# Kernel tuning notes

Measured on AMD Instinct MI355X. Metric: run time of the kernel, lower is better.

The kernel has to match this reference:

```python
import jax, jax.numpy as jnp
import numpy as np

B, DIRS, C, H, W = 2, 64, 630, 128, 128

def setup_inputs() -> dict:
    key = jax.random.key(0)
    k1, k2, k3, k4, k5 = jax.random.split(key, 5)
    theta_global = jax.random.normal(k1, (B, 4, H, W), dtype=jnp.float32) * 0.1
    theta_dir = jax.random.normal(k2, (B, DIRS, 6, H, W), dtype=jnp.float32) * 0.1
    t_vec = jax.random.uniform(k3, (C,), dtype=jnp.float32)
    b_vec = jax.random.uniform(k4, (C,), dtype=jnp.float32)
    P = jax.random.normal(k5, (C, DIRS), dtype=jnp.float32) * 0.1
    return {"theta_global": theta_global, "theta_dir": theta_dir,
            "t_vec": t_vec, "b_vec": b_vec, "P": P}

def _log_s(theta_global, theta_dir, t_vec, b_vec, P):
    ln_s0 = theta_global[:, 0:1]   # [B,1,H,W]
    r = theta_global[:, 1:2]
    sigma20 = theta_global[:, 2:3]
    sigma30 = theta_global[:, 3:4]
    # project all six direction-coefficient maps at once: [B,6,C,H,W]
    proj = jnp.einsum('cd,bdkhw->bkchw', P, theta_dir)
    D_ch, s11, s02, s21, s12, s03 = (proj[:, k] for k in range(6))
    t = t_vec.reshape(1, -1, 1, 1)  # [1,C,1,1]
    b = b_vec.reshape(1, -1, 1, 1)
    t2, b2, tb = t * t, b * b, t * b
    t3, b3, t2b, tb2 = t2 * t, b2 * b, t2 * b, t * b2
    log_s = (ln_s0 - r * t - D_ch * b
             + 0.5 * (sigma20 * t2 + 2.0 * s11 * tb + s02 * b2)
             - (1.0 / 6.0) * (sigma30 * t3 + 3.0 * s21 * t2b + 3.0 * s12 * tb2 + s03 * b3))
    return log_s

def reference(theta_global, theta_dir, t_vec, b_vec, P):
    return jnp.exp(_log_s(theta_global, theta_dir, t_vec, b_vec, P))
```

## Files before the change

### kernel.cpp

```cpp
#include <hip/hip_runtime.h>
#include <math.h>

#define BATCH 2
#define NDIRS 64
#define NCH   630
#define MPAD  640
#define HW    16384
#define KDIR  384
#define NT    12
#define PANEL 64
#define NPOSW 5
#define NITER (NPOSW * NT)
#define BROWE 392

#define BS_OFF 0
#define AS_OFF 50176
#define TV_OFF 74752
#define TG_OFF 77312
#define LDS_TOTAL 78336

typedef float f32x4 __attribute__((ext_vector_type(4)));
typedef short s16x8 __attribute__((ext_vector_type(8)));

__device__ __forceinline__ ushort f2bf(float f) {
    unsigned u = __builtin_bit_cast(unsigned, f);
    u = (u + 0x7FFFu + ((u >> 16) & 1u)) >> 16;
    return (ushort)u;
}

__device__ __forceinline__ uint cvt_pk_bf16(float lo, float hi) {
    uint r;
    asm("v_cvt_pk_bf16_f32 %0, %1, %2" : "=v"(r) : "v"(lo), "v"(hi));
    return r;
}

__device__ __forceinline__ f32x4 ntload(const float* p) {
    return __builtin_nontemporal_load((const f32x4*)p);
}

typedef const __attribute__((address_space(1))) unsigned int g_u32;
typedef __attribute__((address_space(3))) unsigned int l_u32;
__device__ __forceinline__ void gload16(const void* g, void* l) {
    __builtin_amdgcn_global_load_lds((g_u32*)g, (l_u32*)l, 16, 0, 0);
}

__global__ void prep_kernel(const float* __restrict__ t_vec,
                            const float* __restrict__ b_vec,
                            const float* __restrict__ P,
                            ushort* __restrict__ W2b) {
    int c = blockIdx.x;
    int j = threadIdx.x;
    float w = 0.0f;
    if (c < NCH) {
        int d = j / 6, k = j - d * 6;
        float t = t_vec[c];
        float bb = b_vec[c];
        float coeff;
        switch (k) {
            case 0:  coeff = -bb;                           break;
            case 1:  coeff = t * bb;                        break;
            case 2:  coeff = 0.5f * bb * bb;                break;
            case 3:  coeff = -0.5f * t * t * bb;            break;
            case 4:  coeff = -0.5f * t * bb * bb;           break;
            default: coeff = -(1.0f / 6.0f) * bb * bb * bb; break;
        }
        w = coeff * P[c * NDIRS + d];
    }
    int kstep = j >> 5, k5 = j & 31, k8 = k5 >> 3, klo = k5 & 7;
    int s = k8 ^ ((c >> 1) & 3);
    W2b[c * KDIR + kstep * 32 + s * 8 + klo] = f2bf(w);
}

__global__ __launch_bounds__(256, 2) void fused_gemm(
        const ushort* __restrict__ W2b,
        const float*  __restrict__ TD,
        const float*  __restrict__ t_vec,
        const float*  __restrict__ TG,
        float* __restrict__ out)
{
    extern __shared__ char lds[];

    const int nt_ = blockIdx.x;
    const int bz  = blockIdx.y;
    const int n0  = nt_ * PANEL;

    const int tid  = threadIdx.x;
    const int lane = tid & 63;
    const int wid  = tid >> 6;
    const int l15 = lane & 15, lhi = lane >> 4;
    const int aslot = lhi ^ ((l15 >> 1) & 3);

    ushort* bsU = (ushort*)(lds + BS_OFF);
    char*   asW = lds + AS_OFF + wid * 6144;
    float*  tvl = (float*)(lds + TV_OFF);
    float*  tgl = (float*)(lds + TG_OFF);

    tvl[tid]       = t_vec[tid];
    tvl[tid + 256] = t_vec[tid + 256];
    if (tid < NCH - 512) tvl[tid + 512] = t_vec[tid + 512];
    else if (tid + 512 < MPAD) tvl[tid + 512] = 0.0f;
    {
        int p = tid >> 6, px = tid & 63;
        tgl[p * PANEL + px] = TG[((size_t)bz * 4 + p) * HW + n0 + px];
    }

    const ushort* aB0 = W2b + (size_t)(wid * 160 + (lane >> 2)) * KDIR
                        + (lane & 3) * 8;
    const ushort* aB1 = aB0 + (size_t)16 * KDIR;
    gload16(aB0, asW);             gload16(aB1, asW + 1024);
    __builtin_amdgcn_sched_barrier(0);
    gload16(aB0 + 32, asW + 2048); gload16(aB1 + 32, asW + 3072);
    __builtin_amdgcn_sched_barrier(0);

    const int kq2 = tid >> 4;
    const int pg  = tid & 15;
    const float* bR = TD + ((size_t)bz * KDIR + 2 * kq2) * HW + n0 + pg * 4;
    const int sxor = ((kq2 >> 2) ^ (pg & 3) ^ ((pg >> 2) & 3)) & 3;
    const int wbase = (kq2 & 3) * 2;

    {
        f32x4 lo0, hi0, lo1, hi1, lo2, hi2, lo3, hi3;
        lo0 = ntload(bR);
        hi0 = ntload(bR + HW);
        lo1 = ntload(bR + (size_t)32 * HW);
        hi1 = ntload(bR + (size_t)33 * HW);
        lo2 = ntload(bR + (size_t)64 * HW);
        hi2 = ntload(bR + (size_t)65 * HW);

#define BSTEP(S, LC, HC, LN, HN)                                               \
        {                                                                      \
            if ((S) + 3 < NT) {                                                \
                LN = ntload(bR + (size_t)(((S) + 3) * 32) * HW);               \
                HN = ntload(bR + (size_t)(((S) + 3) * 32 + 1) * HW);           \
            }                                                                  \
            _Pragma("unroll")                                                  \
            for (int i = 0; i < 4; ++i) {                                      \
                uint w_ = cvt_pk_bf16(LC[i], HC[i]);                           \
                int s_ = (sxor ^ i) & 3;                                       \
                *(uint*)&bsU[(pg * 4 + i) * BROWE + (S) * 32 + s_ * 8 + wbase] = w_; \
            }                                                                  \
        }
        BSTEP(0, lo0, hi0, lo3, hi3)  BSTEP(1, lo1, hi1, lo0, hi0)
        BSTEP(2, lo2, hi2, lo1, hi1)  BSTEP(3, lo3, hi3, lo2, hi2)
        BSTEP(4, lo0, hi0, lo3, hi3)  BSTEP(5, lo1, hi1, lo0, hi0)
        BSTEP(6, lo2, hi2, lo1, hi1)  BSTEP(7, lo3, hi3, lo2, hi2)
        BSTEP(8, lo0, hi0, lo3, hi3)  BSTEP(9, lo1, hi1, lo0, hi0)
        BSTEP(10, lo2, hi2, lo1, hi1) BSTEP(11, lo3, hi3, lo2, hi2)
#undef BSTEP
    }

    asm volatile("s_waitcnt lgkmcnt(0)" ::: "memory");
    __builtin_amdgcn_s_barrier();
    __builtin_amdgcn_sched_barrier(0);

    float gg[4][4];
    #pragma unroll
    for (int n = 0; n < 4; ++n)
        #pragma unroll
        for (int p = 0; p < 4; ++p) gg[n][p] = tgl[p * PANEL + n * 16 + l15];

    f32x4 acc[2][4];
    #pragma unroll
    for (int m = 0; m < 2; ++m)
        #pragma unroll
        for (int n = 0; n < 4; ++n) acc[m][n] = (f32x4){0.f, 0.f, 0.f, 0.f};

#define ITER(G, WSTR)                                                          \
    {                                                                          \
        constexpr int T_ = (G) % NT, buf_ = (G) % 3;                           \
        constexpr int gn_ = (G) + 2;                                           \
        if constexpr (gn_ < NITER) {                                           \
            constexpr int pi_ = gn_ / NT, ti_ = gn_ % NT, nb_ = gn_ % 3;       \
            gload16(aB0 + (size_t)(pi_ * 32) * KDIR + ti_ * 32,                \
                    asW + nb_ * 2048);                                         \
            gload16(aB1 + (size_t)(pi_ * 32) * KDIR + ti_ * 32,                \
                    asW + nb_ * 2048 + 1024);                                  \
            __builtin_amdgcn_sched_barrier(0);                                 \
        }                                                                      \
        s16x8 bf[4];                                                           \
        _Pragma("unroll")                                                      \
        for (int n = 0; n < 4; ++n) {                                          \
            const int rs_ = (lhi ^ (l15 & 3) ^ ((l15 >> 2) & 3) ^ (n)) & 3;    \
            bf[n] = *(const s16x8*)&bsU[(n * 16 + l15) * BROWE + T_ * 32 + rs_ * 8]; \
        }                                                                      \
        asm volatile(WSTR ::: "memory");                                       \
        s16x8 af[2];                                                           \
        const ushort* asR = (const ushort*)(asW + buf_ * 2048);                \
        _Pragma("unroll")                                                      \
        for (int m = 0; m < 2; ++m)                                            \
            af[m] = *(const s16x8*)&asR[(m * 16 + l15) * 32 + aslot * 8];      \
        __builtin_amdgcn_s_setprio(1);                                         \
        _Pragma("unroll")                                                      \
        for (int m = 0; m < 2; ++m)                                            \
            _Pragma("unroll")                                                  \
            for (int n = 0; n < 4; ++n)                                        \
                acc[m][n] = __builtin_amdgcn_mfma_f32_16x16x32_bf16(           \
                                af[m], bf[n], acc[m][n], 0, 0, 0);             \
        __builtin_amdgcn_s_setprio(0);                                         \
    }

#define EPI(P_)                                                                \
    {                                                                          \
        _Pragma("unroll")                                                      \
        for (int m = 0; m < 2; ++m) {                                          \
            _Pragma("unroll")                                                  \
            for (int r = 0; r < 4; ++r) {                                      \
                int c = wid * 160 + (P_) * 32 + m * 16 + lhi * 4 + r;          \
                float t_ = tvl[c];                                             \
                float ct1 = -t_, ct2 = 0.5f * t_ * t_;                         \
                float ct3 = -(1.0f / 6.0f) * t_ * t_ * t_;                     \
                float* orow = out + ((size_t)bz * NCH + c) * HW + n0 + l15;    \
                _Pragma("unroll")                                              \
                for (int n = 0; n < 4; ++n) {                                  \
                    float base = gg[n][0] + ct1 * gg[n][1]                     \
                               + ct2 * gg[n][2] + ct3 * gg[n][3];              \
                    __builtin_nontemporal_store(                               \
                        __expf(acc[m][n][r] + base), orow + n * 16);           \
                }                                                              \
            }                                                                  \
        }                                                                      \
        _Pragma("unroll")                                                      \
        for (int m = 0; m < 2; ++m)                                            \
            _Pragma("unroll")                                                  \
            for (int n = 0; n < 4; ++n) acc[m][n] = (f32x4){0.f,0.f,0.f,0.f};  \
    }

#define W36 "s_waitcnt vmcnt(36)"
#define W4  "s_waitcnt vmcnt(4)"
#define W2  "s_waitcnt vmcnt(2)"
#define W0  "s_waitcnt vmcnt(0)"

    ITER(0,  W4)  ITER(1,  W4)  ITER(2,  W4)  ITER(3,  W4)  ITER(4,  W4)
    ITER(5,  W4)  ITER(6,  W4)  ITER(7,  W4)  ITER(8,  W4)  ITER(9,  W4)
    ITER(10, W4)  ITER(11, W4)
    EPI(0)
    ITER(12, W36) ITER(13, W36) ITER(14, W4)  ITER(15, W4)  ITER(16, W4)
    ITER(17, W4)  ITER(18, W4)  ITER(19, W4)  ITER(20, W4)  ITER(21, W4)
    ITER(22, W4)  ITER(23, W4)
    EPI(1)
    ITER(24, W36) ITER(25, W36) ITER(26, W4)  ITER(27, W4)  ITER(28, W4)
    ITER(29, W4)  ITER(30, W4)  ITER(31, W4)  ITER(32, W4)  ITER(33, W4)
    ITER(34, W4)  ITER(35, W4)
    EPI(2)
    ITER(36, W36) ITER(37, W36) ITER(38, W4)  ITER(39, W4)  ITER(40, W4)
    ITER(41, W4)  ITER(42, W4)  ITER(43, W4)  ITER(44, W4)  ITER(45, W4)
    ITER(46, W4)  ITER(47, W4)
    EPI(3)
    ITER(48, W36) ITER(49, W36) ITER(50, W4)  ITER(51, W4)  ITER(52, W4)
    ITER(53, W4)  ITER(54, W4)  ITER(55, W4)  ITER(56, W4)  ITER(57, W4)
    ITER(58, W2)  ITER(59, W0)

    {
        #pragma unroll
        for (int m = 0; m < 2; ++m) {
            #pragma unroll
            for (int r = 0; r < 4; ++r) {
                int c = wid * 160 + 4 * 32 + m * 16 + lhi * 4 + r;
                if (c < NCH) {
                    float t_ = tvl[c];
                    float ct1 = -t_, ct2 = 0.5f * t_ * t_;
                    float ct3 = -(1.0f / 6.0f) * t_ * t_ * t_;
                    float* orow = out + ((size_t)bz * NCH + c) * HW + n0 + l15;
                    #pragma unroll
                    for (int n = 0; n < 4; ++n) {
                        float base = gg[n][0] + ct1 * gg[n][1]
                                   + ct2 * gg[n][2] + ct3 * gg[n][3];
                        __builtin_nontemporal_store(
                            __expf(acc[m][n][r] + base), orow + n * 16);
                    }
                }
            }
        }
    }

#undef W36
#undef W4
#undef W2
#undef W0
#undef EPI
#undef ITER
}

extern "C" void kernel_launch(void* const* d_in, const int* in_sizes, int n_in,
                              void* d_out, int out_size, void* d_ws, size_t ws_size,
                              hipStream_t stream) {
    const float* theta_global = (const float*)d_in[0];
    const float* theta_dir    = (const float*)d_in[1];
    const float* t_vec        = (const float*)d_in[2];
    const float* b_vec        = (const float*)d_in[3];
    const float* P            = (const float*)d_in[4];
    float* out = (float*)d_out;

    ushort* W2b = (ushort*)d_ws;

    (void)hipFuncSetAttribute((const void*)fused_gemm,
                              hipFuncAttributeMaxDynamicSharedMemorySize,
                              LDS_TOTAL);

    prep_kernel<<<dim3(MPAD), dim3(KDIR), 0, stream>>>(t_vec, b_vec, P, W2b);
    fused_gemm<<<dim3(HW / PANEL, BATCH), 256, LDS_TOTAL, stream>>>(
        W2b, theta_dir, t_vec, theta_global, out);
}
```

Baseline: 38.85 us.

## Load A-operand fragments directly into registers instead of staging through LDS

The per-wave A tiles (the precomputed bf16 coefficient matrix) were fetched with global_load_lds into a triple-buffered LDS area and then read back from LDS with manual vmcnt waits. They are now loaded straight from global memory into a three-deep register ring (afb) in MFMA fragment layout, and the explicit waitcnt strings are dropped so the compiler inserts them. This removes the LDS round trip and about 24KB of LDS, which can raise occupancy. The cost is more VGPRs, and the compiler-chosen waits may be more conservative, possibly exposing global latency right before the MFMAs.

New measurement: 39.94 us. 2.8% more time.

```diff
diff --git a/kernel.cpp b/kernel.cpp
--- a/kernel.cpp
+++ b/kernel.cpp
@@ -14,10 +14,9 @@
 #define BROWE 392
 
 #define BS_OFF 0
-#define AS_OFF 50176
-#define TV_OFF 74752
-#define TG_OFF 77312
-#define LDS_TOTAL 78336
+#define TV_OFF 50176
+#define TG_OFF 52736
+#define LDS_TOTAL 53760
 
 typedef float f32x4 __attribute__((ext_vector_type(4)));
 typedef short s16x8 __attribute__((ext_vector_type(8)));
@@ -36,12 +35,6 @@
 
 __device__ __forceinline__ f32x4 ntload(const float* p) {
     return __builtin_nontemporal_load((const f32x4*)p);
-}
-
-typedef const __attribute__((address_space(1))) unsigned int g_u32;
-typedef __attribute__((address_space(3))) unsigned int l_u32;
-__device__ __forceinline__ void gload16(const void* g, void* l) {
-    __builtin_amdgcn_global_load_lds((g_u32*)g, (l_u32*)l, 16, 0, 0);
 }
 
 __global__ void prep_kernel(const float* __restrict__ t_vec,
@@ -91,7 +84,6 @@
     const int aslot = lhi ^ ((l15 >> 1) & 3);
 
     ushort* bsU = (ushort*)(lds + BS_OFF);
-    char*   asW = lds + AS_OFF + wid * 6144;
     float*  tvl = (float*)(lds + TV_OFF);
     float*  tgl = (float*)(lds + TG_OFF);
 
@@ -104,12 +96,12 @@
         tgl[p * PANEL + px] = TG[((size_t)bz * 4 + p) * HW + n0 + px];
     }
 
-    const ushort* aB0 = W2b + (size_t)(wid * 160 + (lane >> 2)) * KDIR
-                        + (lane & 3) * 8;
-    const ushort* aB1 = aB0 + (size_t)16 * KDIR;
-    gload16(aB0, asW);             gload16(aB1, asW + 1024);
-    __builtin_amdgcn_sched_barrier(0);
-    gload16(aB0 + 32, asW + 2048); gload16(aB1 + 32, asW + 3072);
+    const ushort* aP = W2b + (wid * 160 + l15) * KDIR + aslot * 8;
+    s16x8 afb[3][2];
+    afb[0][0] = *(const s16x8*)(aP);
+    afb[0][1] = *(const s16x8*)(aP + 16 * KDIR);
+    afb[1][0] = *(const s16x8*)(aP + 32);
+    afb[1][1] = *(const s16x8*)(aP + 16 * KDIR + 32);
     __builtin_amdgcn_sched_barrier(0);
 
     const int kq2 = tid >> 4;
@@ -165,16 +157,15 @@
         #pragma unroll
         for (int n = 0; n < 4; ++n) acc[m][n] = (f32x4){0.f, 0.f, 0.f, 0.f};
 
-#define ITER(G, WSTR)                                                          \
+#define ITER(G)                                                                \
     {                                                                          \
         constexpr int T_ = (G) % NT, buf_ = (G) % 3;                           \
         constexpr int gn_ = (G) + 2;                                           \
         if constexpr (gn_ < NITER) {                                           \
             constexpr int pi_ = gn_ / NT, ti_ = gn_ % NT, nb_ = gn_ % 3;       \
-            gload16(aB0 + (size_t)(pi_ * 32) * KDIR + ti_ * 32,                \
-                    asW + nb_ * 2048);                                         \
-            gload16(aB1 + (size_t)(pi_ * 32) * KDIR + ti_ * 32,                \
-                    asW + nb_ * 2048 + 1024);                                  \
+            afb[nb_][0] = *(const s16x8*)(aP + (pi_ * 32) * KDIR + ti_ * 32);  \
+            afb[nb_][1] = *(const s16x8*)(aP + (pi_ * 32 + 16) * KDIR          \
+                                          + ti_ * 32);                         \
             __builtin_amdgcn_sched_barrier(0);                                 \
         }                                                                      \
         s16x8 bf[4];                                                           \
@@ -183,19 +174,13 @@
             const int rs_ = (lhi ^ (l15 & 3) ^ ((l15 >> 2) & 3) ^ (n)) & 3;    \
             bf[n] = *(const s16x8*)&bsU[(n * 16 + l15) * BROWE + T_ * 32 + rs_ * 8]; \
         }                                                                      \
-        asm volatile(WSTR ::: "memory");                                       \
-        s16x8 af[2];                                                           \
-        const ushort* asR = (const ushort*)(asW + buf_ * 2048);                \
-        _Pragma("unroll")                                                      \
-        for (int m = 0; m < 2; ++m)                                            \
-            af[m] = *(const s16x8*)&asR[(m * 16 + l15) * 32 + aslot * 8];      \
         __builtin_amdgcn_s_setprio(1);                                         \
         _Pragma("unroll")                                                      \
         for (int m = 0; m < 2; ++m)                                            \
             _Pragma("unroll")                                                  \
             for (int n = 0; n < 4; ++n)                                        \
                 acc[m][n] = __builtin_amdgcn_mfma_f32_16x16x32_bf16(           \
-                                af[m], bf[n], acc[m][n], 0, 0, 0);             \
+                                afb[buf_][m], bf[n], acc[m][n], 0, 0, 0);      \
         __builtin_amdgcn_s_setprio(0);                                         \
     }
 
@@ -225,30 +210,20 @@
             for (int n = 0; n < 4; ++n) acc[m][n] = (f32x4){0.f,0.f,0.f,0.f};  \
     }
 
-#define W36 "s_waitcnt vmcnt(36)"
-#define W4  "s_waitcnt vmcnt(4)"
-#define W2  "s_waitcnt vmcnt(2)"
-#define W0  "s_waitcnt vmcnt(0)"
-
-    ITER(0,  W4)  ITER(1,  W4)  ITER(2,  W4)  ITER(3,  W4)  ITER(4,  W4)
-    ITER(5,  W4)  ITER(6,  W4)  ITER(7,  W4)  ITER(8,  W4)  ITER(9,  W4)
-    ITER(10, W4)  ITER(11, W4)
+    ITER(0)  ITER(1)  ITER(2)  ITER(3)  ITER(4)  ITER(5)
+    ITER(6)  ITER(7)  ITER(8)  ITER(9)  ITER(10) ITER(11)
     EPI(0)
-    ITER(12, W36) ITER(13, W36) ITER(14, W4)  ITER(15, W4)  ITER(16, W4)
-    ITER(17, W4)  ITER(18, W4)  ITER(19, W4)  ITER(20, W4)  ITER(21, W4)
-    ITER(22, W4)  ITER(23, W4)
+    ITER(12) ITER(13) ITER(14) ITER(15) ITER(16) ITER(17)
+    ITER(18) ITER(19) ITER(20) ITER(21) ITER(22) ITER(23)
     EPI(1)
-    ITER(24, W36) ITER(25, W36) ITER(26, W4)  ITER(27, W4)  ITER(28, W4)
-    ITER(29, W4)  ITER(30, W4)  ITER(31, W4)  ITER(32, W4)  ITER(33, W4)
-    ITER(34, W4)  ITER(35, W4)
+    ITER(24) ITER(25) ITER(26) ITER(27) ITER(28) ITER(29)
+    ITER(30) ITER(31) ITER(32) ITER(33) ITER(34) ITER(35)
     EPI(2)
-    ITER(36, W36) ITER(37, W36) ITER(38, W4)  ITER(39, W4)  ITER(40, W4)
-    ITER(41, W4)  ITER(42, W4)  ITER(43, W4)  ITER(44, W4)  ITER(45, W4)
-    ITER(46, W4)  ITER(47, W4)
+    ITER(36) ITER(37) ITER(38) ITER(39) ITER(40) ITER(41)
+    ITER(42) ITER(43) ITER(44) ITER(45) ITER(46) ITER(47)
     EPI(3)
-    ITER(48, W36) ITER(49, W36) ITER(50, W4)  ITER(51, W4)  ITER(52, W4)
-    ITER(53, W4)  ITER(54, W4)  ITER(55, W4)  ITER(56, W4)  ITER(57, W4)
-    ITER(58, W2)  ITER(59, W0)
+    ITER(48) ITER(49) ITER(50) ITER(51) ITER(52) ITER(53)
+    ITER(54) ITER(55) ITER(56) ITER(57) ITER(58) ITER(59)
 
     {
         #pragma unroll
@@ -273,10 +248,6 @@
         }
     }
 
-#undef W36
-#undef W4
-#undef W2
-#undef W0
 #undef EPI
 #undef ITER
 }
```
